# Kernel tuning notes

Measured on AMD Instinct MI355X. Metric: run time of the kernel, lower is better.

The kernel has to match this reference:

```python
import jax, jax.numpy as jnp
import numpy as np

B, T, D, H, E = 16, 4096, 256, 512, 8


def setup_inputs() -> dict:
    key = jax.random.key(0)
    ks = jax.random.split(key, 5)
    x = jax.random.normal(ks[0], (B, T, D), dtype=jnp.float32)
    gate_w = jax.random.normal(ks[1], (D, E), dtype=jnp.float32) * 0.02
    gate_b = jnp.zeros((E,), dtype=jnp.float32)
    W1 = jax.random.normal(ks[2], (E, D, H), dtype=jnp.float32) * 0.02
    b1 = jnp.zeros((E, H), dtype=jnp.float32)
    W2 = jax.random.normal(ks[3], (E, H, D), dtype=jnp.float32) * 0.02
    b2 = jnp.zeros((E, D), dtype=jnp.float32)
    return {"x": x, "gate_w": gate_w, "gate_b": gate_b,
            "W1": W1, "b1": b1, "W2": W2, "b2": b2}


def reference(x, gate_w, gate_b, W1, b1, W2, b2):
    Bb, Tt, Dd = x.shape
    Ee = gate_w.shape[1]
    xf = x.reshape(-1, Dd)                       # [N, D]
    N = xf.shape[0]
    logits = xf @ gate_w + gate_b                # [N, E]
    probs = jax.nn.softmax(logits, axis=-1)
    top2_vals, top2_idx = jax.lax.top_k(probs, 2)  # [N, 2]
    # combine weights: w[n, e] = sum_k top2_vals[n,k] * (top2_idx[n,k]==e)
    cw = jnp.zeros((N, Ee), dtype=xf.dtype).at[
        jnp.arange(N)[:, None], top2_idx].add(top2_vals)  # [N, E]

    def step(acc, params):
        w1, bb1, w2, bb2, we = params            # per-expert slices
        h = jax.nn.gelu(xf @ w1 + bb1, approximate=False)  # [N, H]
        y = h @ w2 + bb2                          # [N, D]
        return acc + we[:, None] * y, None

    out, _ = jax.lax.scan(step, jnp.zeros_like(xf),
                          (W1, b1, W2, b2, cw.T))
    return out.reshape(Bb, Tt, Dd)
```

## Files before the change

kernel.cpp:

```cpp
#include <hip/hip_runtime.h>
#include <hip/hip_bf16.h>
#include <math.h>


#define N_TOK 65536
#define D_DIM 256
#define H_DIM 512
#define TILE_R 32
#define GRID_TILES 2112

typedef __bf16 bf16x8 __attribute__((ext_vector_type(8)));
typedef float f32x4 __attribute__((ext_vector_type(4)));

static __device__ __forceinline__ ushort f2bf(float f) {
    __hip_bfloat16 h = __float2bfloat16(f);
    ushort u;
    __builtin_memcpy(&u, &h, 2);
    return u;
}

static __device__ __forceinline__ float gelu(float v) {
    const float a = fabsf(v) * 0.70710678118654752f;
    const float t = __builtin_amdgcn_rcpf(fmaf(a, 0.47047f, 1.0f));
    const float p = t * fmaf(t, fmaf(t, 0.7478556f, -0.0958798f), 0.3480242f);
    const float er = fmaf(-p, __expf(-a * a), 1.0f);
    const float s = copysignf(er, v);
    return 0.5f * v * (1.0f + s);
}

__global__ __launch_bounds__(256) void prep(const float* __restrict__ x,
                                            const float* __restrict__ gate_w,
                                            const float* __restrict__ gate_b,
                                            const float* __restrict__ W1,
                                            const float* __restrict__ W2,
                                            ushort* __restrict__ xb,
                                            ushort* __restrict__ W1p,
                                            ushort* __restrict__ W2p,
                                            int* __restrict__ counts,
                                            int* __restrict__ pid_arr,
                                            float2* __restrict__ pw_arr) {
    __shared__ float gws[2048];
    __shared__ int lc[64];

    const int bid = blockIdx.x;
    const int tid = threadIdx.x;

    if (bid >= 1024) {
        const int pid = bid - 1024;
        const int t = (pid & 511) * 256 + tid;
        const int l = t & 63;
        const int lo = l & 15, hi = l >> 4;
        ushort v[8];
        if (pid < 512) {
            const int kb = (t >> 6) & 7;
            const int nb = (t >> 9) & 31;
            const int e  = t >> 14;
            const int k0 = kb * 32 + hi * 8;
            const int n  = nb * 16 + lo;
            const float* src = W1 + (size_t)e * D_DIM * H_DIM + n;
            #pragma unroll
            for (int j = 0; j < 8; ++j)
                v[j] = f2bf(src[(size_t)(k0 + j) * H_DIM]);
            *(uint4*)(W1p + (size_t)t * 8) = *(const uint4*)v;
        } else {
            const int kb = (t >> 6) & 15;
            const int nb = (t >> 10) & 15;
            const int e  = t >> 14;
            const int k0 = kb * 32 + hi * 8;
            const int n  = nb * 16 + lo;
            const float* src = W2 + (size_t)e * H_DIM * D_DIM + n;
            #pragma unroll
            for (int j = 0; j < 8; ++j)
                v[j] = f2bf(src[(size_t)(k0 + j) * D_DIM]);
            *(uint4*)(W2p + (size_t)t * 8) = *(const uint4*)v;
        }
        return;
    }

    const size_t t0 = (size_t)bid * 64;
    for (int i = tid; i < 2048; i += 256) gws[i] = gate_w[i];
    if (tid < 64) lc[tid] = 0;
    __syncthreads();

    const int m = tid >> 2, q = tid & 3;
    const float4* xr = (const float4*)(x + (t0 + m) * D_DIM + q * 64);
    ushort4* xw = (ushort4*)(xb + (t0 + m) * D_DIM + q * 64);

    double lg[8] = {0, 0, 0, 0, 0, 0, 0, 0};
    #pragma unroll
    for (int it = 0; it < 16; ++it) {
        const float4 v = xr[it];
        ushort4 bv;
        bv.x = f2bf(v.x); bv.y = f2bf(v.y); bv.z = f2bf(v.z); bv.w = f2bf(v.w);
        xw[it] = bv;
        const float* g = &gws[(q * 64 + it * 4) * 8];
        const float vv[4] = {v.x, v.y, v.z, v.w};
        #pragma unroll
        for (int j = 0; j < 4; ++j) {
            const double xv = (double)vv[j];
            #pragma unroll
            for (int e2 = 0; e2 < 8; ++e2) lg[e2] += xv * (double)g[j * 8 + e2];
        }
    }
    #pragma unroll
    for (int e2 = 0; e2 < 8; ++e2) {
        lg[e2] += __shfl_xor(lg[e2], 1, 64);
        lg[e2] += __shfl_xor(lg[e2], 2, 64);
    }

    if (q == 0) {
        int e0 = 0, e1 = -1;
        #pragma unroll
        for (int e2 = 0; e2 < 8; ++e2) lg[e2] += (double)gate_b[e2];
        double b0 = -1e300, b1v = -1e300;
        #pragma unroll
        for (int e2 = 0; e2 < 8; ++e2)
            if (lg[e2] > b0) { b0 = lg[e2]; e0 = e2; }
        #pragma unroll
        for (int e2 = 0; e2 < 8; ++e2)
            if (e2 != e0 && lg[e2] > b1v) { b1v = lg[e2]; e1 = e2; }
        double s = 0;
        #pragma unroll
        for (int e2 = 0; e2 < 8; ++e2) s += exp(lg[e2] - b0);
        const float p0 = (float)(1.0 / s);
        const float p1 = (float)(exp(b1v - b0) / s);
        const int pid = e0 * 8 + e1;
        atomicAdd(&lc[pid], 1);
        const int tok = (int)t0 + m;
        pid_arr[tok] = pid;
        pw_arr[tok] = make_float2(p0, p1);
    }
    __syncthreads();
    if (tid < 64 && lc[tid]) atomicAdd(&counts[tid], lc[tid]);
}

__global__ __launch_bounds__(256) void scatter(const int* __restrict__ counts,
                                               const int* __restrict__ pid_arr,
                                               const float2* __restrict__ pw_arr,
                                               int* __restrict__ cursor,
                                               int* __restrict__ tok_list,
                                               float* __restrict__ w0l,
                                               float* __restrict__ w1l) {
    __shared__ int lcnt[64];
    __shared__ int lbase[64];
    const int tid = threadIdx.x;
    const int t = blockIdx.x * 256 + tid;
    if (tid < 64) lcnt[tid] = 0;
    __syncthreads();
    const int pid = pid_arr[t];
    const float2 pw = pw_arr[t];
    const int lpos = atomicAdd(&lcnt[pid], 1);
    __syncthreads();
    if (tid < 64) {
        int s = 0;
        for (int i = 0; i < tid; ++i) s += counts[i];
        const int mine = lcnt[tid];
        lbase[tid] = s + (mine ? atomicAdd(&cursor[tid], mine) : 0);
    }
    __syncthreads();
    const int pos = lbase[pid] + lpos;
    tok_list[pos] = t;
    w0l[pos] = pw.x;
    w1l[pos] = pw.y;
}

__global__ __launch_bounds__(512, 3) void moe_expert(const ushort* __restrict__ xb,
                                                     const ushort* __restrict__ W1p,
                                                     const ushort* __restrict__ W2p,
                                                     const float* __restrict__ b1,
                                                     const float* __restrict__ b2,
                                                     const int* __restrict__ counts,
                                                     const int* __restrict__ tok_list,
                                                     const float* __restrict__ w0l,
                                                     const float* __restrict__ w1l,
                                                     float* __restrict__ out) {
    __shared__ __align__(16) char Xs[TILE_R * 512];
    __shared__ __align__(16) char Hs[TILE_R * 2048];

    int n = 0;
    for (int i = 0; i < 64; ++i) n += (counts[i] + 31) >> 5;
    const int qn = n >> 3, rn = n & 7;
    const int xc = blockIdx.x & 7, ix = blockIdx.x >> 3;
    if (ix >= qn + (xc < rn ? 1 : 0)) return;
    const int wg = xc * qn + min(xc, rn) + ix;

    int pid = -1, row0 = 0, nv = 0, gbase = 0;
    int st = 0, sc = 0;
    for (int i = 0; i < 64; ++i) {
        const int c = counts[i];
        const int nt = (c + 31) >> 5;
        if (pid < 0 && wg < st + nt) { pid = i; row0 = (wg - st) << 5; nv = min(TILE_R, c - row0); gbase = sc; }
        st += nt; sc += c;
    }
    const int ea = pid >> 3, eb = pid & 7;
    const int gidx = gbase + row0;

    const int tid = threadIdx.x;
    const int w = tid >> 6, l = tid & 63;
    const int lo = l & 15, hi = l >> 4;
    const int qe = w >> 2, pp = w & 3;
    const int ew = qe ? eb : ea;

    const float* wl = qe ? w1l : w0l;
    const float wtv0 = wl[gidx + min(lo, nv - 1)];
    const float wtv1 = wl[gidx + min(16 + lo, nv - 1)];

    {
        const int r = tid >> 4;
        const int tk = tok_list[gidx + min(r, nv - 1)];
        const char* src = (const char*)(xb + (size_t)tk * D_DIM) + (tid & 15) * 32;
        const int bo = (tid & 15) * 32, sw = (r & 7) << 4;
        const uint4 a0 = *(const uint4*)src;
        const uint4 a1 = *(const uint4*)(src + 16);
        *(uint4*)(Xs + r * 512 + (bo ^ sw)) = a0;
        *(uint4*)(Xs + r * 512 + ((bo + 16) ^ sw)) = a1;
    }
    __syncthreads();

    #pragma unroll
    for (int hh = 0; hh < 2; ++hh) {
        const int nbg0 = pp * 8 + hh * 4;
        const char* w1b = (const char*)W1p + (size_t)(ew * 32 + nbg0) * 8192 + (size_t)l * 16;

        f32x4 acc1[4][2];
        #pragma unroll
        for (int nb = 0; nb < 4; ++nb)
            #pragma unroll
            for (int tb = 0; tb < 2; ++tb)
                acc1[nb][tb] = (f32x4){0.f, 0.f, 0.f, 0.f};

        bf16x8 wf[2][4];
        #pragma unroll
        for (int nb = 0; nb < 4; ++nb)
            wf[0][nb] = *(const bf16x8*)(w1b + nb * 8192);

        #pragma unroll
        for (int ks = 0; ks < 8; ++ks) {
            const int cb = ks & 1, nx = cb ^ 1;
            if (ks < 7) {
                #pragma unroll
                for (int nb = 0; nb < 4; ++nb)
                    wf[nx][nb] = *(const bf16x8*)(w1b + nb * 8192 + (ks + 1) * 1024);
            }
            #pragma unroll
            for (int tb = 0; tb < 2; ++tb) {
                const int slot = tb * 16 + lo;
                const bf16x8 xf = *(const bf16x8*)(Xs + slot * 512 +
                                  ((ks * 64 + hi * 16) ^ ((slot & 7) << 4)));
                __builtin_amdgcn_s_setprio(1);
                #pragma unroll
                for (int nb = 0; nb < 4; ++nb)
                    acc1[nb][tb] = __builtin_amdgcn_mfma_f32_16x16x32_bf16(wf[cb][nb], xf, acc1[nb][tb], 0, 0, 0);
                __builtin_amdgcn_s_setprio(0);
            }
        }

        #pragma unroll
        for (int nb = 0; nb < 4; ++nb) {
            const int hc = nbg0 * 16 + nb * 16 + hi * 4;
            const float4 b1q = *(const float4*)(b1 + ew * H_DIM + hc);
            const int hgc = qe * H_DIM + hc;
            #pragma unroll
            for (int tb = 0; tb < 2; ++tb) {
                const int slot = tb * 16 + lo;
                const float wt = tb ? wtv1 : wtv0;
                ushort4 hv;
                hv.x = f2bf(gelu(acc1[nb][tb][0] + b1q.x) * wt);
                hv.y = f2bf(gelu(acc1[nb][tb][1] + b1q.y) * wt);
                hv.z = f2bf(gelu(acc1[nb][tb][2] + b1q.z) * wt);
                hv.w = f2bf(gelu(acc1[nb][tb][3] + b1q.w) * wt);
                *(ushort4*)(Hs + slot * 2048 + ((hgc * 2) ^ ((slot & 7) << 4))) = hv;
            }
        }
    }
    __syncthreads();

    const char* w2A = (const char*)W2p + (size_t)(ea * 16 + w * 2) * 16384 + (size_t)l * 16;
    const char* w2B = (const char*)W2p + (size_t)(eb * 16 + w * 2) * 16384 + (size_t)l * 16;

    f32x4 acc2[2][2];
    #pragma unroll
    for (int mi = 0; mi < 2; ++mi)
        #pragma unroll
        for (int ni = 0; ni < 2; ++ni)
            acc2[mi][ni] = (f32x4){0.f, 0.f, 0.f, 0.f};

    bf16x8 wf2[3][2];
    #pragma unroll
    for (int ni = 0; ni < 2; ++ni) {
        wf2[0][ni] = *(const bf16x8*)(w2A + ni * 16384);
        wf2[1][ni] = *(const bf16x8*)(w2A + ni * 16384 + 1024);
    }

    #pragma unroll
    for (int ks = 0; ks < 32; ++ks) {
        const int cb = ks % 3;
        if (ks < 30) {
            const int lb = (ks + 2) % 3;
            const int kk = ks + 2;
            const char* base = (kk < 16) ? w2A : w2B;
            const int kloc = kk & 15;
            wf2[lb][0] = *(const bf16x8*)(base + kloc * 1024);
            wf2[lb][1] = *(const bf16x8*)(base + 16384 + kloc * 1024);
        }
        #pragma unroll
        for (int mi = 0; mi < 2; ++mi) {
            const int slot = mi * 16 + lo;
            const bf16x8 hf = *(const bf16x8*)(Hs + slot * 2048 +
                              ((ks * 64 + hi * 16) ^ ((slot & 7) << 4)));
            __builtin_amdgcn_s_setprio(1);
            #pragma unroll
            for (int ni = 0; ni < 2; ++ni)
                acc2[mi][ni] = __builtin_amdgcn_mfma_f32_16x16x32_bf16(hf, wf2[cb][ni], acc2[mi][ni], 0, 0, 0);
            __builtin_amdgcn_s_setprio(0);
        }
    }

    #pragma unroll
    for (int ni = 0; ni < 2; ++ni) {
        const int col = w * 32 + ni * 16 + lo;
        const float b2a = b2[ea * D_DIM + col];
        const float b2b = b2[eb * D_DIM + col];
        #pragma unroll
        for (int mi = 0; mi < 2; ++mi) {
            #pragma unroll
            for (int rg = 0; rg < 4; ++rg) {
                const int r = mi * 16 + hi * 4 + rg;
                if (r < nv) {
                    const int tok = tok_list[gidx + r];
                    const float v = acc2[mi][ni][rg] + w0l[gidx + r] * b2a + w1l[gidx + r] * b2b;
                    out[(size_t)tok * D_DIM + col] = v;
                }
            }
        }
    }
}

extern "C" void kernel_launch(void* const* d_in, const int* in_sizes, int n_in,
                              void* d_out, int out_size, void* d_ws, size_t ws_size,
                              hipStream_t stream) {
    const float* x      = (const float*)d_in[0];
    const float* gate_w = (const float*)d_in[1];
    const float* gate_b = (const float*)d_in[2];
    const float* W1     = (const float*)d_in[3];
    const float* b1     = (const float*)d_in[4];
    const float* W2     = (const float*)d_in[5];
    const float* b2     = (const float*)d_in[6];
    float* out = (float*)d_out;

    char* ws = (char*)d_ws;
    ushort* xb      = (ushort*)(ws);
    ushort* W1p     = (ushort*)(ws + 33554432);
    ushort* W2p     = (ushort*)(ws + 35651584);
    int*    pid_arr = (int*)   (ws + 37748736);
    float2* pw_arr  = (float2*)(ws + 38010880);
    int*    tok_lst = (int*)   (ws + 38535168);
    float*  w0l     = (float*) (ws + 38797312);
    float*  w1l     = (float*) (ws + 39059456);
    int*    counts  = (int*)   (ws + 39321600);
    int*    cursor  = (int*)   (ws + 39321856);

    hipMemsetAsync(counts, 0, 512, stream);

    prep<<<dim3(2048), 256, 0, stream>>>(x, gate_w, gate_b, W1, W2,
                                         xb, W1p, W2p, counts, pid_arr, pw_arr);
    scatter<<<dim3(256), 256, 0, stream>>>(counts, pid_arr, pw_arr, cursor,
                                           tok_lst, w0l, w1l);
    moe_expert<<<dim3(GRID_TILES), 512, 0, stream>>>(xb, W1p, W2p, b1, b2, counts,
                                                     tok_lst, w0l, w1l, out);
}
```

Baseline: 207.7 us.

## Process two experts sequentially to halve LDS and double expert-kernel occupancy

The expert kernel now handles the two experts of a pair one after another instead of splitting waves across them. Each phase computes a half-size H tile (32x512) in shared memory and accumulates the second GEMM across both phases, which halves the Hs buffer and allows launch bounds of 6 blocks per CU. Token indices and combine weights are cached in shared memory. The prep kernel also uses 32 tokens per block with an 8-way shuffle reduction for more gating parallelism. The cost is an extra barrier pair and serialized per-expert phases within each block.

New measurement: 230.2 us. 10.8% more time.

```diff
diff --git a/kernel.cpp b/kernel.cpp
--- a/kernel.cpp
+++ b/kernel.cpp
@@ -45,8 +45,8 @@
     const int bid = blockIdx.x;
     const int tid = threadIdx.x;
 
-    if (bid >= 1024) {
-        const int pid = bid - 1024;
+    if (bid >= 2048) {
+        const int pid = bid - 2048;
         const int t = (pid & 511) * 256 + tid;
         const int l = t & 63;
         const int lo = l & 15, hi = l >> 4;
@@ -77,23 +77,23 @@
         return;
     }
 
-    const size_t t0 = (size_t)bid * 64;
+    const size_t t0 = (size_t)bid * 32;
     for (int i = tid; i < 2048; i += 256) gws[i] = gate_w[i];
     if (tid < 64) lc[tid] = 0;
     __syncthreads();
 
-    const int m = tid >> 2, q = tid & 3;
-    const float4* xr = (const float4*)(x + (t0 + m) * D_DIM + q * 64);
-    ushort4* xw = (ushort4*)(xb + (t0 + m) * D_DIM + q * 64);
+    const int m = tid >> 3, q = tid & 7;
+    const float4* xr = (const float4*)(x + (t0 + m) * D_DIM + q * 32);
+    ushort4* xw = (ushort4*)(xb + (t0 + m) * D_DIM + q * 32);
 
     double lg[8] = {0, 0, 0, 0, 0, 0, 0, 0};
     #pragma unroll
-    for (int it = 0; it < 16; ++it) {
+    for (int it = 0; it < 8; ++it) {
         const float4 v = xr[it];
         ushort4 bv;
         bv.x = f2bf(v.x); bv.y = f2bf(v.y); bv.z = f2bf(v.z); bv.w = f2bf(v.w);
         xw[it] = bv;
-        const float* g = &gws[(q * 64 + it * 4) * 8];
+        const float* g = &gws[(q * 32 + it * 4) * 8];
         const float vv[4] = {v.x, v.y, v.z, v.w};
         #pragma unroll
         for (int j = 0; j < 4; ++j) {
@@ -106,6 +106,7 @@
     for (int e2 = 0; e2 < 8; ++e2) {
         lg[e2] += __shfl_xor(lg[e2], 1, 64);
         lg[e2] += __shfl_xor(lg[e2], 2, 64);
+        lg[e2] += __shfl_xor(lg[e2], 4, 64);
     }
 
     if (q == 0) {
@@ -164,7 +165,7 @@
     w1l[pos] = pw.y;
 }
 
-__global__ __launch_bounds__(512, 3) void moe_expert(const ushort* __restrict__ xb,
+__global__ __launch_bounds__(512, 6) void moe_expert(const ushort* __restrict__ xb,
                                                      const ushort* __restrict__ W1p,
                                                      const ushort* __restrict__ W2p,
                                                      const float* __restrict__ b1,
@@ -175,7 +176,9 @@
                                                      const float* __restrict__ w1l,
                                                      float* __restrict__ out) {
     __shared__ __align__(16) char Xs[TILE_R * 512];
-    __shared__ __align__(16) char Hs[TILE_R * 2048];
+    __shared__ __align__(16) char Hs[TILE_R * 1024];
+    __shared__ int   toks[TILE_R];
+    __shared__ float wgt[2][TILE_R];
 
     int n = 0;
     for (int i = 0; i < 64; ++i) n += (counts[i] + 31) >> 5;
@@ -198,12 +201,14 @@
     const int tid = threadIdx.x;
     const int w = tid >> 6, l = tid & 63;
     const int lo = l & 15, hi = l >> 4;
-    const int qe = w >> 2, pp = w & 3;
-    const int ew = qe ? eb : ea;
-
-    const float* wl = qe ? w1l : w0l;
-    const float wtv0 = wl[gidx + min(lo, nv - 1)];
-    const float wtv1 = wl[gidx + min(16 + lo, nv - 1)];
+
+    if (tid < TILE_R) {
+        const bool vld = tid < nv;
+        const int src = gidx + (vld ? tid : 0);
+        toks[tid]   = tok_list[src];
+        wgt[0][tid] = vld ? w0l[src] : 0.f;
+        wgt[1][tid] = vld ? w1l[src] : 0.f;
+    }
 
     {
         const int r = tid >> 4;
@@ -217,103 +222,105 @@
     }
     __syncthreads();
 
-    #pragma unroll
-    for (int hh = 0; hh < 2; ++hh) {
-        const int nbg0 = pp * 8 + hh * 4;
-        const char* w1b = (const char*)W1p + (size_t)(ew * 32 + nbg0) * 8192 + (size_t)l * 16;
-
-        f32x4 acc1[4][2];
-        #pragma unroll
-        for (int nb = 0; nb < 4; ++nb)
-            #pragma unroll
-            for (int tb = 0; tb < 2; ++tb)
-                acc1[nb][tb] = (f32x4){0.f, 0.f, 0.f, 0.f};
-
-        bf16x8 wf[2][4];
-        #pragma unroll
-        for (int nb = 0; nb < 4; ++nb)
-            wf[0][nb] = *(const bf16x8*)(w1b + nb * 8192);
-
-        #pragma unroll
-        for (int ks = 0; ks < 8; ++ks) {
-            const int cb = ks & 1, nx = cb ^ 1;
-            if (ks < 7) {
+    f32x4 acc2[2][2];
+    #pragma unroll
+    for (int mi = 0; mi < 2; ++mi)
+        #pragma unroll
+        for (int ni = 0; ni < 2; ++ni)
+            acc2[mi][ni] = (f32x4){0.f, 0.f, 0.f, 0.f};
+
+    #pragma unroll
+    for (int ph = 0; ph < 2; ++ph) {
+        const int ew = ph ? eb : ea;
+
+        #pragma unroll
+        for (int pass = 0; pass < 2; ++pass) {
+            const int nb0 = w * 4 + pass * 2;
+            const char* w1b = (const char*)W1p + (size_t)(ew * 32 + nb0) * 8192 + (size_t)l * 16;
+
+            f32x4 acc1[2][2];
+            #pragma unroll
+            for (int nb = 0; nb < 2; ++nb)
                 #pragma unroll
-                for (int nb = 0; nb < 4; ++nb)
-                    wf[nx][nb] = *(const bf16x8*)(w1b + nb * 8192 + (ks + 1) * 1024);
-            }
-            #pragma unroll
-            for (int tb = 0; tb < 2; ++tb) {
-                const int slot = tb * 16 + lo;
-                const bf16x8 xf = *(const bf16x8*)(Xs + slot * 512 +
+                for (int tb = 0; tb < 2; ++tb)
+                    acc1[nb][tb] = (f32x4){0.f, 0.f, 0.f, 0.f};
+
+            bf16x8 wf[3][2];
+            #pragma unroll
+            for (int nb = 0; nb < 2; ++nb) {
+                wf[0][nb] = *(const bf16x8*)(w1b + nb * 8192);
+                wf[1][nb] = *(const bf16x8*)(w1b + nb * 8192 + 1024);
+            }
+
+            #pragma unroll
+            for (int ks = 0; ks < 8; ++ks) {
+                const int cb = ks % 3;
+                if (ks < 6) {
+                    const int lb = (ks + 2) % 3;
+                    wf[lb][0] = *(const bf16x8*)(w1b + (ks + 2) * 1024);
+                    wf[lb][1] = *(const bf16x8*)(w1b + 8192 + (ks + 2) * 1024);
+                }
+                #pragma unroll
+                for (int tb = 0; tb < 2; ++tb) {
+                    const int slot = tb * 16 + lo;
+                    const bf16x8 xf = *(const bf16x8*)(Xs + slot * 512 +
+                                      ((ks * 64 + hi * 16) ^ ((slot & 7) << 4)));
+                    __builtin_amdgcn_s_setprio(1);
+                    #pragma unroll
+                    for (int nb = 0; nb < 2; ++nb)
+                        acc1[nb][tb] = __builtin_amdgcn_mfma_f32_16x16x32_bf16(wf[cb][nb], xf, acc1[nb][tb], 0, 0, 0);
+                    __builtin_amdgcn_s_setprio(0);
+                }
+            }
+
+            #pragma unroll
+            for (int nb = 0; nb < 2; ++nb) {
+                const int hc = (nb0 + nb) * 16 + hi * 4;
+                const float4 b1q = *(const float4*)(b1 + ew * H_DIM + hc);
+                #pragma unroll
+                for (int tb = 0; tb < 2; ++tb) {
+                    const int slot = tb * 16 + lo;
+                    const float wt = wgt[ph][slot];
+                    ushort4 hv;
+                    hv.x = f2bf(gelu(acc1[nb][tb][0] + b1q.x) * wt);
+                    hv.y = f2bf(gelu(acc1[nb][tb][1] + b1q.y) * wt);
+                    hv.z = f2bf(gelu(acc1[nb][tb][2] + b1q.z) * wt);
+                    hv.w = f2bf(gelu(acc1[nb][tb][3] + b1q.w) * wt);
+                    *(ushort4*)(Hs + slot * 1024 + ((hc * 2) ^ ((slot & 7) << 4))) = hv;
+                }
+            }
+        }
+        __syncthreads();
+
+        const char* w2b = (const char*)W2p + (size_t)(ew * 16 + w * 2) * 16384 + (size_t)l * 16;
+        bf16x8 wf2[3][2];
+        #pragma unroll
+        for (int ni = 0; ni < 2; ++ni) {
+            wf2[0][ni] = *(const bf16x8*)(w2b + ni * 16384);
+            wf2[1][ni] = *(const bf16x8*)(w2b + ni * 16384 + 1024);
+        }
+
+        #pragma unroll
+        for (int ks = 0; ks < 16; ++ks) {
+            const int cb = ks % 3;
+            if (ks < 14) {
+                const int lb = (ks + 2) % 3;
+                wf2[lb][0] = *(const bf16x8*)(w2b + (ks + 2) * 1024);
+                wf2[lb][1] = *(const bf16x8*)(w2b + 16384 + (ks + 2) * 1024);
+            }
+            #pragma unroll
+            for (int mi = 0; mi < 2; ++mi) {
+                const int slot = mi * 16 + lo;
+                const bf16x8 hf = *(const bf16x8*)(Hs + slot * 1024 +
                                   ((ks * 64 + hi * 16) ^ ((slot & 7) << 4)));
                 __builtin_amdgcn_s_setprio(1);
                 #pragma unroll
-                for (int nb = 0; nb < 4; ++nb)
-                    acc1[nb][tb] = __builtin_amdgcn_mfma_f32_16x16x32_bf16(wf[cb][nb], xf, acc1[nb][tb], 0, 0, 0);
+                for (int ni = 0; ni < 2; ++ni)
+                    acc2[mi][ni] = __builtin_amdgcn_mfma_f32_16x16x32_bf16(hf, wf2[cb][ni], acc2[mi][ni], 0, 0, 0);
                 __builtin_amdgcn_s_setprio(0);
             }
         }
-
-        #pragma unroll
-        for (int nb = 0; nb < 4; ++nb) {
-            const int hc = nbg0 * 16 + nb * 16 + hi * 4;
-            const float4 b1q = *(const float4*)(b1 + ew * H_DIM + hc);
-            const int hgc = qe * H_DIM + hc;
-            #pragma unroll
-            for (int tb = 0; tb < 2; ++tb) {
-                const int slot = tb * 16 + lo;
-                const float wt = tb ? wtv1 : wtv0;
-                ushort4 hv;
-                hv.x = f2bf(gelu(acc1[nb][tb][0] + b1q.x) * wt);
-                hv.y = f2bf(gelu(acc1[nb][tb][1] + b1q.y) * wt);
-                hv.z = f2bf(gelu(acc1[nb][tb][2] + b1q.z) * wt);
-                hv.w = f2bf(gelu(acc1[nb][tb][3] + b1q.w) * wt);
-                *(ushort4*)(Hs + slot * 2048 + ((hgc * 2) ^ ((slot & 7) << 4))) = hv;
-            }
-        }
-    }
-    __syncthreads();
-
-    const char* w2A = (const char*)W2p + (size_t)(ea * 16 + w * 2) * 16384 + (size_t)l * 16;
-    const char* w2B = (const char*)W2p + (size_t)(eb * 16 + w * 2) * 16384 + (size_t)l * 16;
-
-    f32x4 acc2[2][2];
-    #pragma unroll
-    for (int mi = 0; mi < 2; ++mi)
-        #pragma unroll
-        for (int ni = 0; ni < 2; ++ni)
-            acc2[mi][ni] = (f32x4){0.f, 0.f, 0.f, 0.f};
-
-    bf16x8 wf2[3][2];
-    #pragma unroll
-    for (int ni = 0; ni < 2; ++ni) {
-        wf2[0][ni] = *(const bf16x8*)(w2A + ni * 16384);
-        wf2[1][ni] = *(const bf16x8*)(w2A + ni * 16384 + 1024);
-    }
-
-    #pragma unroll
-    for (int ks = 0; ks < 32; ++ks) {
-        const int cb = ks % 3;
-        if (ks < 30) {
-            const int lb = (ks + 2) % 3;
-            const int kk = ks + 2;
-            const char* base = (kk < 16) ? w2A : w2B;
-            const int kloc = kk & 15;
-            wf2[lb][0] = *(const bf16x8*)(base + kloc * 1024);
-            wf2[lb][1] = *(const bf16x8*)(base + 16384 + kloc * 1024);
-        }
-        #pragma unroll
-        for (int mi = 0; mi < 2; ++mi) {
-            const int slot = mi * 16 + lo;
-            const bf16x8 hf = *(const bf16x8*)(Hs + slot * 2048 +
-                              ((ks * 64 + hi * 16) ^ ((slot & 7) << 4)));
-            __builtin_amdgcn_s_setprio(1);
-            #pragma unroll
-            for (int ni = 0; ni < 2; ++ni)
-                acc2[mi][ni] = __builtin_amdgcn_mfma_f32_16x16x32_bf16(hf, wf2[cb][ni], acc2[mi][ni], 0, 0, 0);
-            __builtin_amdgcn_s_setprio(0);
-        }
+        if (ph == 0) __syncthreads();
     }
 
     #pragma unroll
@@ -327,9 +334,8 @@
             for (int rg = 0; rg < 4; ++rg) {
                 const int r = mi * 16 + hi * 4 + rg;
                 if (r < nv) {
-                    const int tok = tok_list[gidx + r];
-                    const float v = acc2[mi][ni][rg] + w0l[gidx + r] * b2a + w1l[gidx + r] * b2b;
-                    out[(size_t)tok * D_DIM + col] = v;
+                    const float v = acc2[mi][ni][rg] + wgt[0][r] * b2a + wgt[1][r] * b2b;
+                    out[(size_t)toks[r] * D_DIM + col] = v;
                 }
             }
         }
@@ -362,7 +368,7 @@
 
     hipMemsetAsync(counts, 0, 512, stream);
 
-    prep<<<dim3(2048), 256, 0, stream>>>(x, gate_w, gate_b, W1, W2,
+    prep<<<dim3(3072), 256, 0, stream>>>(x, gate_w, gate_b, W1, W2,
                                          xb, W1p, W2p, counts, pid_arr, pw_arr);
     scatter<<<dim3(256), 256, 0, stream>>>(counts, pid_arr, pw_arr, cursor,
                                            tok_lst, w0l, w1l);
```
